# Performance work log

Measured on AMD Instinct MI355X. Metric: run time of the kernel, lower is better.

Reference implementation:

```python
import jax, jax.numpy as jnp
import numpy as np

# dims
B, S, H = 2, 256, 1024          # batch, global seq, global hidden
BH, NH = 384, 8                  # byte_hidden, num heads
HD = BH // NH                    # head dim = 48
P = 4                            # num_global_proj (seed byte positions)
S_C = 12                         # byte decode steps (= target.shape[2])
L = 4                            # num_byte_decoder_layers
V = 258                          # byte vocab (256 bytes + pad 256 + eos 257)
T = P + S_C
EOS = 257
SCALE = 1.0 / np.sqrt(HD)


def setup_inputs() -> dict:
    key = jax.random.key(0)
    ks = jax.random.split(key, 12)
    w = lambda k, shp: jax.random.normal(k, shp, jnp.float32) * 0.02
    return {
        "x": jax.random.normal(ks[0], (B, S, H), jnp.float32),
        "target": jax.random.randint(ks[1], (B, S, S_C), 0, V),
        "Wproj": w(ks[2], (H, P * BH)),
        "attn_norm": jnp.ones((L, BH), jnp.float32),
        "Wq": w(ks[3], (L, BH, BH)),
        "Wk": w(ks[4], (L, BH, BH)),
        "Wv": w(ks[5], (L, BH, BH)),
        "Wo": w(ks[6], (L, BH, BH)),
        "ffn_norm": jnp.ones((L, BH), jnp.float32),
        "W1": w(ks[7], (L, BH, 4 * BH)),
        "W2": w(ks[8], (L, 4 * BH, BH)),
        "Wlm": w(ks[9], (BH, V)),
    }


def _rms(x, g):
    return x * jax.lax.rsqrt(jnp.mean(x * x, -1, keepdims=True) + 1e-5) * g


def _block(x, kc, vc, pos, an, Wq, Wk, Wv, Wo, fn, W1, W2, causal):
    # x: [N, Lq, BH]; kc/vc: [N, T, NH, HD] KV caches; pos: static write offset
    N, Lq, _ = x.shape
    h = _rms(x, an)
    q = (h @ Wq).reshape(N, Lq, NH, HD)
    k = (h @ Wk).reshape(N, Lq, NH, HD)
    v = (h @ Wv).reshape(N, Lq, NH, HD)
    kc = jax.lax.dynamic_update_slice(kc, k, (0, pos, 0, 0))
    vc = jax.lax.dynamic_update_slice(vc, v, (0, pos, 0, 0))
    nk = pos + Lq
    sc = jnp.einsum('nqhd,nkhd->nhqk', q, kc[:, :nk]) * SCALE
    if causal:
        mask = jnp.arange(nk)[None, :] <= (pos + jnp.arange(Lq))[:, None]
        sc = jnp.where(mask[None, None], sc, jnp.float32(-1e30))
    p = jax.nn.softmax(sc, axis=-1)
    o = jnp.einsum('nhqk,nkhd->nqhd', p, vc[:, :nk]).reshape(N, Lq, BH)
    x = x + o @ Wo
    x = x + jax.nn.gelu(_rms(x, fn) @ W1, approximate=False) @ W2
    return x, kc, vc


def _forward(x, Wproj, attn_norm, Wq, Wk, Wv, Wo, ffn_norm, W1, W2, Wlm):
    N = B * S
    x0 = (x.reshape(N, H) @ Wproj).reshape(N, P, BH)
    x_out = jnp.zeros((N, T, BH), x0.dtype).at[:, :P].set(x0)
    kc = [jnp.zeros((N, T, NH, HD), x0.dtype) for _ in range(L)]
    vc = [jnp.zeros((N, T, NH, HD), x0.dtype) for _ in range(L)]
    finished = jnp.zeros((N,), bool)
    for i in range(S_C):
        if i == 0:
            pos, xi, causal = 0, x_out[:, :P], True          # prefill seed bytes
        else:
            pos, xi, causal = P + i - 1, x_out[:, P + i - 1:P + i], False  # decode 1 token
        for l in range(L):
            xi, kc[l], vc[l] = _block(xi, kc[l], vc[l], pos,
                                      attn_norm[l], Wq[l], Wk[l], Wv[l], Wo[l],
                                      ffn_norm[l], W1[l], W2[l], causal)
        gen = xi[:, -1]                                       # [N, BH]
        unf = ~finished
        # scatter only unfinished streams back (finished stay zero, as in torch)
        x_out = x_out.at[:, P + i].set(jnp.where(unf[:, None], gen, jnp.float32(0.0)))
        finished = finished | (unf & (jnp.argmax(gen, -1) == EOS))
    return x_out.reshape(B, S, T, BH)[:, :, P:, :] @ Wlm      # [B,S,S_C,V]


def reference(x, target, Wproj, attn_norm, Wq, Wk, Wv, Wo, ffn_norm, W1, W2, Wlm):
    del target  # only sets S_c (static here)
    return _forward(x, Wproj, attn_norm, Wq, Wk, Wv, Wo, ffn_norm, W1, W2, Wlm)
```

## Files before the change

kernel.cpp:

```cpp
#include <hip/hip_runtime.h>
#include <hip/hip_bf16.h>


constexpr int H_IN  = 1024;
constexpr int BH    = 384;
constexpr int NH    = 8;
constexpr int HD    = 48;
constexpr int PP    = 4;
constexpr int S_CNT = 12;
constexpr int NL    = 4;
constexpr int NV    = 258;
constexpr int TT    = 16;
constexpr int NSEQ  = 512;
constexpr int EOS_I = 257;
constexpr int NTH   = 768;
constexpr float RSCALE = 0.14433756729740646f;

typedef _Float16 h2 __attribute__((ext_vector_type(2)));
typedef _Float16 h8 __attribute__((ext_vector_type(8)));

union W16 { h8 v8; h2 h[4]; _Float16 e[8]; };

template<int N> struct IC { static constexpr int value = N; };

__device__ __forceinline__ float fdot2(h2 a, h2 b, float c) {
#if __has_builtin(__builtin_amdgcn_fdot2)
  return __builtin_amdgcn_fdot2(a, b, c, false);
#else
  return c + (float)a.x * (float)b.x + (float)a.y * (float)b.y;
#endif
}

__global__ __launch_bounds__(256)
void pack8_kernel(const float* __restrict__ src, const float* __restrict__ g,
                  h8* __restrict__ dst, int C) {
  int c  = blockIdx.x * 256 + threadIdx.x;
  int j8 = blockIdx.y;
  if (c < C) {
    h8 v;
    #pragma unroll
    for (int r = 0; r < 8; r++) {
      int row = 8 * j8 + r;
      float s = g ? g[row] : 1.0f;
      v[r] = (_Float16)(src[(size_t)row * C + c] * s);
    }
    dst[(size_t)j8 * C + c] = v;
  }
}

__global__ __launch_bounds__(NTH)
void decoder_kernel(const float* __restrict__ x,
                    const h8* __restrict__ Wproj8,
                    const h8* __restrict__ Wq8,
                    const h8* __restrict__ Wk8,
                    const h8* __restrict__ Wv8,
                    const h8* __restrict__ Wo8,
                    const h8* __restrict__ W18,
                    const h8* __restrict__ W28,
                    const h8* __restrict__ Wlm8,
                    float* __restrict__ out,
                    _Float16* __restrict__ kbuf,
                    _Float16* __restrict__ vbuf)
{
  __shared__ float xs[2][4][BH];
  __shared__ __align__(16) _Float16 xh[2][4][BH];
  __shared__ __align__(16) _Float16 qh[2][4][BH];
  __shared__ __align__(16) _Float16 oh[2][4][BH];
  __shared__ float sc[2][NH][4][TT];
  __shared__ __align__(16) union Scr {
    float qkvp[3][2][4][BH];
    float wop[2][4][BH];
    struct { __align__(16) _Float16 f1h[2][4][4*BH];
             float w2p[2][4][BH]; } ffn;
    __align__(16) _Float16 xin[2][H_IN];
  } scr;
  __shared__ float redsq[2][4][6];
  __shared__ float redv[12];
  __shared__ int   redi[12];
  __shared__ int   fin[2];

  const int tid = threadIdx.x;
  const int kg  = tid / BH;
  const int col = tid - kg * BH;
  const int sq  = kg;
  const int wid = tid >> 6;
  const int w6  = wid % 6;
  const int seq0 = blockIdx.x * 2;

  if (tid < 2) fin[tid] = 0;

  for (int s = 0; s < 2; s++) {
    const size_t base = (size_t)(seq0 + s) * H_IN;
    for (int j = tid; j < H_IN; j += NTH) scr.xin[s][j] = (_Float16)x[base + j];
  }
  __syncthreads();
  {
    float acc[2][2] = {};
    for (int j8 = 0; j8 < H_IN / 8; j8 += 4) {
      W16 w0[4], w1[4];
      #pragma unroll
      for (int u = 0; u < 4; u++) {
        w0[u].v8 = Wproj8[(size_t)(j8 + u) * (PP * BH) + tid];
        w1[u].v8 = Wproj8[(size_t)(j8 + u) * (PP * BH) + tid + NTH];
      }
      #pragma unroll
      for (int u = 0; u < 4; u++)
        #pragma unroll
        for (int s = 0; s < 2; s++) {
          W16 hv; hv.v8 = *(const h8*)&scr.xin[s][(j8 + u) * 8];
          #pragma unroll
          for (int r = 0; r < 4; r++) {
            acc[s][0] = fdot2(hv.h[r], w0[u].h[r], acc[s][0]);
            acc[s][1] = fdot2(hv.h[r], w1[u].h[r], acc[s][1]);
          }
        }
    }
    const int m0 = tid / BH, cc = tid - m0 * BH;
    #pragma unroll
    for (int s = 0; s < 2; s++) {
      xs[s][m0][cc]     = acc[s][0];  xh[s][m0][cc]     = (_Float16)acc[s][0];
      xs[s][m0 + 2][cc] = acc[s][1];  xh[s][m0 + 2][cc] = (_Float16)acc[s][1];
      float r0 = acc[s][0] * acc[s][0], r1 = acc[s][1] * acc[s][1];
      #pragma unroll
      for (int off = 32; off; off >>= 1) {
        r0 += __shfl_down(r0, off, 64); r1 += __shfl_down(r1, off, 64);
      }
      if ((tid & 63) == 0) { redsq[s][m0][w6] = r0; redsq[s][m0 + 2][w6] = r1; }
    }
  }
  __syncthreads();

  auto layers = [&](auto ntc, int pos, bool causal) {
    constexpr int NT = decltype(ntc)::value;
    const int nk = pos + NT;
    for (int l = 0; l < NL; l++) {
      {
        const size_t wb = ((size_t)l * 48 + kg * 24) * BH + col;
        float aq[2][NT] = {}, ak[2][NT] = {}, av[2][NT] = {};
        for (int j8 = 0; j8 < 24; j8 += 4) {
          W16 wq[4], wk[4], wv[4];
          #pragma unroll
          for (int u = 0; u < 4; u++) {
            wq[u].v8 = Wq8[wb + (size_t)(j8 + u) * BH];
            wk[u].v8 = Wk8[wb + (size_t)(j8 + u) * BH];
            wv[u].v8 = Wv8[wb + (size_t)(j8 + u) * BH];
          }
          #pragma unroll
          for (int u = 0; u < 4; u++)
            #pragma unroll
            for (int s = 0; s < 2; s++)
              #pragma unroll
              for (int tok = 0; tok < NT; tok++) {
                W16 hv; hv.v8 = *(const h8*)&xh[s][tok][(kg * 24 + j8 + u) * 8];
                #pragma unroll
                for (int r = 0; r < 4; r++) {
                  aq[s][tok] = fdot2(hv.h[r], wq[u].h[r], aq[s][tok]);
                  ak[s][tok] = fdot2(hv.h[r], wk[u].h[r], ak[s][tok]);
                  av[s][tok] = fdot2(hv.h[r], wv[u].h[r], av[s][tok]);
                }
              }
        }
        if (kg == 1) {
          #pragma unroll
          for (int s = 0; s < 2; s++)
            #pragma unroll
            for (int tok = 0; tok < NT; tok++) {
              scr.qkvp[0][s][tok][col] = aq[s][tok];
              scr.qkvp[1][s][tok][col] = ak[s][tok];
              scr.qkvp[2][s][tok][col] = av[s][tok];
            }
        }
        __syncthreads();
        if (kg == 0) {
          #pragma unroll
          for (int s = 0; s < 2; s++) {
            const size_t cb = (((size_t)(seq0 + s) * NL + l) * TT + pos) * BH + col;
            #pragma unroll
            for (int tok = 0; tok < NT; tok++) {
              float ss = redsq[s][tok][0] + redsq[s][tok][1] + redsq[s][tok][2] +
                         redsq[s][tok][3] + redsq[s][tok][4] + redsq[s][tok][5];
              float sca = rsqrtf(ss * (1.0f / BH) + 1e-5f);
              qh[s][tok][col] = (_Float16)((aq[s][tok] + scr.qkvp[0][s][tok][col]) * sca * RSCALE);
              kbuf[cb + (size_t)tok * BH] = (_Float16)((ak[s][tok] + scr.qkvp[1][s][tok][col]) * sca);
              vbuf[cb + (size_t)tok * BH] = (_Float16)((av[s][tok] + scr.qkvp[2][s][tok][col]) * sca);
            }
          }
        }
        __syncthreads();
      }
      {
        const int nu = 2 * NH * NT * nk;
        if (tid < nu) {
          int s = tid / (NH * NT * nk), r = tid % (NH * NT * nk);
          int h = r / (NT * nk); int r2 = r % (NT * nk);
          int qi = r2 / nk, j = r2 % nk;
          float d;
          if (causal && j > pos + qi) d = -1e30f;
          else {
            const h8* kp8 = (const h8*)(kbuf + (((size_t)(seq0 + s) * NL + l) * TT + j) * BH + h * HD);
            W16 kk[6];
            #pragma unroll
            for (int c = 0; c < 6; c++) kk[c].v8 = kp8[c];
            d = 0.f;
            #pragma unroll
            for (int c = 0; c < 6; c++)
              #pragma unroll
              for (int e = 0; e < 8; e++)
                d += (float)qh[s][qi][h * HD + c * 8 + e] * (float)kk[c].e[e];
          }
          sc[s][h][qi][j] = d;
        }
      }
      __syncthreads();
      {
        const int nr = 2 * NH * NT;
        if (tid < nr) {
          int s = tid / (NH * NT), r = tid % (NH * NT);
          int h = r / NT, qi = r % NT;
          float m = -3.0e38f;
          for (int j = 0; j < nk; j++) m = fmaxf(m, sc[s][h][qi][j]);
          float den = 0.f;
          for (int j = 0; j < nk; j++) {
            float e = expf(sc[s][h][qi][j] - m);
            sc[s][h][qi][j] = e; den += e;
          }
          float inv = 1.0f / den;
          for (int j = 0; j < nk; j++) sc[s][h][qi][j] *= inv;
        }
      }
      __syncthreads();
      {
        const size_t vb = (((size_t)(seq0 + sq) * NL + l) * TT) * BH + col;
        const int h = col / HD;
        #pragma unroll
        for (int tok = 0; tok < NT; tok++) {
          float acc = 0.f;
          int j = 0;
          for (; j + 4 <= nk; j += 4) {
            float v0 = (float)vbuf[vb + (size_t)(j + 0) * BH];
            float v1 = (float)vbuf[vb + (size_t)(j + 1) * BH];
            float v2 = (float)vbuf[vb + (size_t)(j + 2) * BH];
            float v3 = (float)vbuf[vb + (size_t)(j + 3) * BH];
            acc += sc[sq][h][tok][j] * v0 + sc[sq][h][tok][j+1] * v1 +
                   sc[sq][h][tok][j+2] * v2 + sc[sq][h][tok][j+3] * v3;
          }
          for (; j < nk; j++)
            acc += sc[sq][h][tok][j] * (float)vbuf[vb + (size_t)j * BH];
          oh[sq][tok][col] = (_Float16)acc;
        }
      }
      __syncthreads();
      {
        const size_t wb = ((size_t)l * 48 + kg * 24) * BH + col;
        float ao[2][NT] = {};
        for (int j8 = 0; j8 < 24; j8 += 8) {
          W16 w[8];
          #pragma unroll
          for (int u = 0; u < 8; u++) w[u].v8 = Wo8[wb + (size_t)(j8 + u) * BH];
          #pragma unroll
          for (int u = 0; u < 8; u++)
            #pragma unroll
            for (int s = 0; s < 2; s++)
              #pragma unroll
              for (int tok = 0; tok < NT; tok++) {
                W16 hv; hv.v8 = *(const h8*)&oh[s][tok][(kg * 24 + j8 + u) * 8];
                #pragma unroll
                for (int r = 0; r < 4; r++)
                  ao[s][tok] = fdot2(hv.h[r], w[u].h[r], ao[s][tok]);
              }
        }
        if (kg == 1) {
          #pragma unroll
          for (int s = 0; s < 2; s++)
            #pragma unroll
            for (int tok = 0; tok < NT; tok++) scr.wop[s][tok][col] = ao[s][tok];
        }
        __syncthreads();
        if (kg == 0) {
          #pragma unroll
          for (int s = 0; s < 2; s++)
            #pragma unroll
            for (int tok = 0; tok < NT; tok++) {
              float xn = xs[s][tok][col] + ao[s][tok] + scr.wop[s][tok][col];
              xs[s][tok][col] = xn; xh[s][tok][col] = (_Float16)xn;
              float r = xn * xn;
              #pragma unroll
              for (int off = 32; off; off >>= 1) r += __shfl_down(r, off, 64);
              if ((tid & 63) == 0) redsq[s][tok][wid] = r;
            }
        }
        __syncthreads();
      }
      {
        float a1[2][NT][2] = {};
        for (int j8 = 0; j8 < 48; j8 += 4) {
          W16 w0[4], w1[4];
          #pragma unroll
          for (int u = 0; u < 4; u++) {
            w0[u].v8 = W18[((size_t)(l * 48 + j8 + u)) * (4 * BH) + tid];
            w1[u].v8 = W18[((size_t)(l * 48 + j8 + u)) * (4 * BH) + tid + NTH];
          }
          #pragma unroll
          for (int u = 0; u < 4; u++)
            #pragma unroll
            for (int s = 0; s < 2; s++)
              #pragma unroll
              for (int t = 0; t < NT; t++) {
                W16 hv; hv.v8 = *(const h8*)&xh[s][t][(j8 + u) * 8];
                #pragma unroll
                for (int r = 0; r < 4; r++) {
                  a1[s][t][0] = fdot2(hv.h[r], w0[u].h[r], a1[s][t][0]);
                  a1[s][t][1] = fdot2(hv.h[r], w1[u].h[r], a1[s][t][1]);
                }
              }
        }
        #pragma unroll
        for (int s = 0; s < 2; s++)
          #pragma unroll
          for (int t = 0; t < NT; t++) {
            float ss = redsq[s][t][0] + redsq[s][t][1] + redsq[s][t][2] +
                       redsq[s][t][3] + redsq[s][t][4] + redsq[s][t][5];
            float sca = rsqrtf(ss * (1.0f / BH) + 1e-5f);
            float z0 = a1[s][t][0] * sca, z1 = a1[s][t][1] * sca;
            scr.ffn.f1h[s][t][tid]       = (_Float16)(0.5f * z0 * (1.0f + erff(z0 * 0.7071067811865476f)));
            scr.ffn.f1h[s][t][tid + NTH] = (_Float16)(0.5f * z1 * (1.0f + erff(z1 * 0.7071067811865476f)));
          }
        __syncthreads();
        {
          float a2[2][NT] = {};
          for (int j8 = 0; j8 < 96; j8 += 8) {
            W16 w[8];
            #pragma unroll
            for (int u = 0; u < 8; u++)
              w[u].v8 = W28[((size_t)(l * 192 + kg * 96 + j8 + u)) * BH + col];
            #pragma unroll
            for (int u = 0; u < 8; u++)
              #pragma unroll
              for (int s = 0; s < 2; s++)
                #pragma unroll
                for (int t = 0; t < NT; t++) {
                  W16 fv; fv.v8 = *(const h8*)&scr.ffn.f1h[s][t][(kg * 96 + j8 + u) * 8];
                  #pragma unroll
                  for (int r = 0; r < 4; r++)
                    a2[s][t] = fdot2(fv.h[r], w[u].h[r], a2[s][t]);
                }
          }
          if (kg == 1) {
            #pragma unroll
            for (int s = 0; s < 2; s++)
              #pragma unroll
              for (int t = 0; t < NT; t++) scr.ffn.w2p[s][t][col] = a2[s][t];
          }
          __syncthreads();
          if (kg == 0) {
            #pragma unroll
            for (int s = 0; s < 2; s++)
              #pragma unroll
              for (int t = 0; t < NT; t++) {
                float xn = xs[s][t][col] + a2[s][t] + scr.ffn.w2p[s][t][col];
                xs[s][t][col] = xn; xh[s][t][col] = (_Float16)xn;
                float r = xn * xn;
                #pragma unroll
                for (int off = 32; off; off >>= 1) r += __shfl_down(r, off, 64);
                if ((tid & 63) == 0) redsq[s][t][wid] = r;
              }
          }
          __syncthreads();
        }
      }
    }
  };

  for (int i = 0; i < S_CNT; i++) {
    int grow;
    if (i == 0) { layers(IC<4>{}, 0, true);           grow = 3; }
    else        { layers(IC<1>{}, PP + i - 1, false); grow = 0; }

    {
      float gen = xs[sq][grow][col];
      float v = gen; int idx = col;
      #pragma unroll
      for (int off = 32; off; off >>= 1) {
        float v2 = __shfl_down(v, off, 64); int i2 = __shfl_down(idx, off, 64);
        if (v2 > v || (v2 == v && i2 < idx)) { v = v2; idx = i2; }
      }
      if ((tid & 63) == 0) { redv[wid] = v; redi[wid] = idx; }
      float nxt = fin[sq] ? 0.0f : gen;
      xs[sq][0][col] = nxt; xh[sq][0][col] = (_Float16)nxt;
      float r = nxt * nxt;
      #pragma unroll
      for (int off = 32; off; off >>= 1) r += __shfl_down(r, off, 64);
      if ((tid & 63) == 0) redsq[sq][0][w6] = r;
      __syncthreads();
    }
    {
      if (col == 0) {
        const int b = sq * 6;
        float bv = redv[b]; int bi = redi[b];
        for (int w = 1; w < 6; w++)
          if (redv[b + w] > bv || (redv[b + w] == bv && redi[b + w] < bi)) {
            bv = redv[b + w]; bi = redi[b + w];
          }
        if (bi == EOS_I) fin[sq] = 1;
      }
      if (col < NV) {
        float acc = 0.f;
        for (int j8 = 0; j8 < 48; j8 += 8) {
          W16 w[8];
          #pragma unroll
          for (int u = 0; u < 8; u++) w[u].v8 = Wlm8[(size_t)(j8 + u) * NV + col];
          #pragma unroll
          for (int u = 0; u < 8; u++) {
            W16 gv; gv.v8 = *(const h8*)&xh[sq][0][(j8 + u) * 8];
            #pragma unroll
            for (int r = 0; r < 4; r++) acc = fdot2(gv.h[r], w[u].h[r], acc);
          }
        }
        out[((size_t)(seq0 + sq) * S_CNT + i) * NV + col] = acc;
      }
      __syncthreads();
    }
  }
}

extern "C" void kernel_launch(void* const* d_in, const int* in_sizes, int n_in,
                              void* d_out, int out_size, void* d_ws, size_t ws_size,
                              hipStream_t stream) {
  const float* x     = (const float*)d_in[0];
  const float* Wproj = (const float*)d_in[2];
  const float* an    = (const float*)d_in[3];
  const float* Wq    = (const float*)d_in[4];
  const float* Wk    = (const float*)d_in[5];
  const float* Wv    = (const float*)d_in[6];
  const float* Wo    = (const float*)d_in[7];
  const float* fn    = (const float*)d_in[8];
  const float* W1    = (const float*)d_in[9];
  const float* W2    = (const float*)d_in[10];
  const float* Wlm   = (const float*)d_in[11];
  float* out = (float*)d_out;
  (void)ws_size; (void)in_sizes; (void)n_in; (void)out_size;

  h8* w = (h8*)d_ws;
  const int n_proj = (H_IN / 8) * (PP * BH);
  const int n_qkvo = NL * (BH / 8) * BH;
  const int n_w1   = NL * (BH / 8) * (4 * BH);
  const int n_w2   = NL * (4 * BH / 8) * BH;
  const int n_lm   = (BH / 8) * NV;
  h8* Wproj_p = w;  w += n_proj;
  h8* Wq_p    = w;  w += n_qkvo;
  h8* Wk_p    = w;  w += n_qkvo;
  h8* Wv_p    = w;  w += n_qkvo;
  h8* Wo_p    = w;  w += n_qkvo;
  h8* W1_p    = w;  w += n_w1;
  h8* W2_p    = w;  w += n_w2;
  h8* Wlm_p   = w;  w += n_lm;
  const size_t kv_elems = (size_t)NSEQ * NL * TT * BH;
  _Float16* kbuf = (_Float16*)w;
  _Float16* vbuf = kbuf + kv_elems;

  auto pack = [&](const float* src, const float* g, h8* dst, int R, int C) {
    dim3 grid((C + 255) / 256, R / 8);
    pack8_kernel<<<grid, 256, 0, stream>>>(src, g, dst, C);
  };
  pack(Wproj, nullptr, Wproj_p, H_IN,        PP * BH);
  pack(Wq,    an,      Wq_p,    NL * BH,     BH);
  pack(Wk,    an,      Wk_p,    NL * BH,     BH);
  pack(Wv,    an,      Wv_p,    NL * BH,     BH);
  pack(Wo,    nullptr, Wo_p,    NL * BH,     BH);
  pack(W1,    fn,      W1_p,    NL * BH,     4 * BH);
  pack(W2,    nullptr, W2_p,    NL * 4 * BH, BH);
  pack(Wlm,   nullptr, Wlm_p,   BH,          NV);

  decoder_kernel<<<NSEQ / 2, NTH, 0, stream>>>(
      x, Wproj_p, Wq_p, Wk_p, Wv_p, Wo_p, W1_p, W2_p, Wlm_p, out, kbuf, vbuf);
}
```

Before: 2.422 ms.

## Double-buffer weight loads, split partial-sum epilogues, fuse decode attention softmax

Every weight-streaming GEMV loop (Wproj, QKV, Wo, W1, W2, Wlm) now software-pipelines its global loads into a two-stage register buffer, so the next chunk is fetched while the current one is multiplied. The split-K epilogues let each half-block finish one sequence instead of half the threads idling while the other half does both. For single-token decode, score computation and softmax are fused into one phase using 16-lane shuffles, which removes a barrier and the serial per-row softmax loop. The cost is higher register pressure from the doubled weight buffers and full unrolling.

After: 7.653 ms. 3.16x slower.

```diff
diff --git a/kernel.cpp b/kernel.cpp
--- a/kernel.cpp
+++ b/kernel.cpp
@@ -96,22 +96,31 @@
   __syncthreads();
   {
     float acc[2][2] = {};
-    for (int j8 = 0; j8 < H_IN / 8; j8 += 4) {
-      W16 w0[4], w1[4];
-      #pragma unroll
-      for (int u = 0; u < 4; u++) {
-        w0[u].v8 = Wproj8[(size_t)(j8 + u) * (PP * BH) + tid];
-        w1[u].v8 = Wproj8[(size_t)(j8 + u) * (PP * BH) + tid + NTH];
+    W16 b0[2][4], b1[2][4];
+    #pragma unroll
+    for (int u = 0; u < 4; u++) {
+      b0[0][u].v8 = Wproj8[(size_t)u * (PP * BH) + tid];
+      b1[0][u].v8 = Wproj8[(size_t)u * (PP * BH) + tid + NTH];
+    }
+    #pragma unroll
+    for (int c = 0; c < 32; c++) {
+      const int cur = c & 1, nxt = cur ^ 1;
+      if (c < 31) {
+        #pragma unroll
+        for (int u = 0; u < 4; u++) {
+          b0[nxt][u].v8 = Wproj8[(size_t)((c + 1) * 4 + u) * (PP * BH) + tid];
+          b1[nxt][u].v8 = Wproj8[(size_t)((c + 1) * 4 + u) * (PP * BH) + tid + NTH];
+        }
       }
       #pragma unroll
       for (int u = 0; u < 4; u++)
         #pragma unroll
         for (int s = 0; s < 2; s++) {
-          W16 hv; hv.v8 = *(const h8*)&scr.xin[s][(j8 + u) * 8];
+          W16 hv; hv.v8 = *(const h8*)&scr.xin[s][(c * 4 + u) * 8];
           #pragma unroll
           for (int r = 0; r < 4; r++) {
-            acc[s][0] = fdot2(hv.h[r], w0[u].h[r], acc[s][0]);
-            acc[s][1] = fdot2(hv.h[r], w1[u].h[r], acc[s][1]);
+            acc[s][0] = fdot2(hv.h[r], b0[cur][u].h[r], acc[s][0]);
+            acc[s][1] = fdot2(hv.h[r], b1[cur][u].h[r], acc[s][1]);
           }
         }
     }
@@ -137,13 +146,24 @@
       {
         const size_t wb = ((size_t)l * 48 + kg * 24) * BH + col;
         float aq[2][NT] = {}, ak[2][NT] = {}, av[2][NT] = {};
-        for (int j8 = 0; j8 < 24; j8 += 4) {
-          W16 wq[4], wk[4], wv[4];
-          #pragma unroll
-          for (int u = 0; u < 4; u++) {
-            wq[u].v8 = Wq8[wb + (size_t)(j8 + u) * BH];
-            wk[u].v8 = Wk8[wb + (size_t)(j8 + u) * BH];
-            wv[u].v8 = Wv8[wb + (size_t)(j8 + u) * BH];
+        W16 bq[2][4], bk[2][4], bv[2][4];
+        #pragma unroll
+        for (int u = 0; u < 4; u++) {
+          bq[0][u].v8 = Wq8[wb + (size_t)u * BH];
+          bk[0][u].v8 = Wk8[wb + (size_t)u * BH];
+          bv[0][u].v8 = Wv8[wb + (size_t)u * BH];
+        }
+        #pragma unroll
+        for (int c = 0; c < 6; c++) {
+          const int cur = c & 1, nxt = cur ^ 1;
+          if (c < 5) {
+            #pragma unroll
+            for (int u = 0; u < 4; u++) {
+              const size_t j = (size_t)((c + 1) * 4 + u) * BH;
+              bq[nxt][u].v8 = Wq8[wb + j];
+              bk[nxt][u].v8 = Wk8[wb + j];
+              bv[nxt][u].v8 = Wv8[wb + j];
+            }
           }
           #pragma unroll
           for (int u = 0; u < 4; u++)
@@ -151,84 +171,109 @@
             for (int s = 0; s < 2; s++)
               #pragma unroll
               for (int tok = 0; tok < NT; tok++) {
-                W16 hv; hv.v8 = *(const h8*)&xh[s][tok][(kg * 24 + j8 + u) * 8];
+                W16 hv; hv.v8 = *(const h8*)&xh[s][tok][(kg * 24 + c * 4 + u) * 8];
                 #pragma unroll
                 for (int r = 0; r < 4; r++) {
-                  aq[s][tok] = fdot2(hv.h[r], wq[u].h[r], aq[s][tok]);
-                  ak[s][tok] = fdot2(hv.h[r], wk[u].h[r], ak[s][tok]);
-                  av[s][tok] = fdot2(hv.h[r], wv[u].h[r], av[s][tok]);
+                  aq[s][tok] = fdot2(hv.h[r], bq[cur][u].h[r], aq[s][tok]);
+                  ak[s][tok] = fdot2(hv.h[r], bk[cur][u].h[r], ak[s][tok]);
+                  av[s][tok] = fdot2(hv.h[r], bv[cur][u].h[r], av[s][tok]);
                 }
               }
         }
-        if (kg == 1) {
-          #pragma unroll
-          for (int s = 0; s < 2; s++)
-            #pragma unroll
-            for (int tok = 0; tok < NT; tok++) {
-              scr.qkvp[0][s][tok][col] = aq[s][tok];
-              scr.qkvp[1][s][tok][col] = ak[s][tok];
-              scr.qkvp[2][s][tok][col] = av[s][tok];
-            }
-        }
-        __syncthreads();
-        if (kg == 0) {
-          #pragma unroll
-          for (int s = 0; s < 2; s++) {
-            const size_t cb = (((size_t)(seq0 + s) * NL + l) * TT + pos) * BH + col;
-            #pragma unroll
-            for (int tok = 0; tok < NT; tok++) {
-              float ss = redsq[s][tok][0] + redsq[s][tok][1] + redsq[s][tok][2] +
-                         redsq[s][tok][3] + redsq[s][tok][4] + redsq[s][tok][5];
-              float sca = rsqrtf(ss * (1.0f / BH) + 1e-5f);
-              qh[s][tok][col] = (_Float16)((aq[s][tok] + scr.qkvp[0][s][tok][col]) * sca * RSCALE);
-              kbuf[cb + (size_t)tok * BH] = (_Float16)((ak[s][tok] + scr.qkvp[1][s][tok][col]) * sca);
-              vbuf[cb + (size_t)tok * BH] = (_Float16)((av[s][tok] + scr.qkvp[2][s][tok][col]) * sca);
-            }
-          }
-        }
-        __syncthreads();
-      }
-      {
-        const int nu = 2 * NH * NT * nk;
-        if (tid < nu) {
-          int s = tid / (NH * NT * nk), r = tid % (NH * NT * nk);
-          int h = r / (NT * nk); int r2 = r % (NT * nk);
-          int qi = r2 / nk, j = r2 % nk;
-          float d;
-          if (causal && j > pos + qi) d = -1e30f;
-          else {
+        {
+          const int so = kg ^ 1;
+          #pragma unroll
+          for (int tok = 0; tok < NT; tok++) {
+            scr.qkvp[0][so][tok][col] = aq[so][tok];
+            scr.qkvp[1][so][tok][col] = ak[so][tok];
+            scr.qkvp[2][so][tok][col] = av[so][tok];
+          }
+        }
+        __syncthreads();
+        {
+          const int s = kg;
+          const size_t cb = (((size_t)(seq0 + s) * NL + l) * TT + pos) * BH + col;
+          #pragma unroll
+          for (int tok = 0; tok < NT; tok++) {
+            float ss = redsq[s][tok][0] + redsq[s][tok][1] + redsq[s][tok][2] +
+                       redsq[s][tok][3] + redsq[s][tok][4] + redsq[s][tok][5];
+            float sca = rsqrtf(ss * (1.0f / BH) + 1e-5f);
+            qh[s][tok][col] = (_Float16)((aq[s][tok] + scr.qkvp[0][s][tok][col]) * sca * RSCALE);
+            kbuf[cb + (size_t)tok * BH] = (_Float16)((ak[s][tok] + scr.qkvp[1][s][tok][col]) * sca);
+            vbuf[cb + (size_t)tok * BH] = (_Float16)((av[s][tok] + scr.qkvp[2][s][tok][col]) * sca);
+          }
+        }
+        __syncthreads();
+      }
+      if constexpr (NT == 1) {
+        if (tid < 2 * NH * TT) {
+          const int s = tid >> 7, r = tid & 127, h = r >> 4, j = r & 15;
+          float d = -1e30f;
+          if (j < nk) {
             const h8* kp8 = (const h8*)(kbuf + (((size_t)(seq0 + s) * NL + l) * TT + j) * BH + h * HD);
-            W16 kk[6];
-            #pragma unroll
-            for (int c = 0; c < 6; c++) kk[c].v8 = kp8[c];
             d = 0.f;
             #pragma unroll
-            for (int c = 0; c < 6; c++)
-              #pragma unroll
-              for (int e = 0; e < 8; e++)
-                d += (float)qh[s][qi][h * HD + c * 8 + e] * (float)kk[c].e[e];
-          }
-          sc[s][h][qi][j] = d;
-        }
-      }
-      __syncthreads();
-      {
-        const int nr = 2 * NH * NT;
-        if (tid < nr) {
-          int s = tid / (NH * NT), r = tid % (NH * NT);
-          int h = r / NT, qi = r % NT;
-          float m = -3.0e38f;
-          for (int j = 0; j < nk; j++) m = fmaxf(m, sc[s][h][qi][j]);
-          float den = 0.f;
-          for (int j = 0; j < nk; j++) {
-            float e = expf(sc[s][h][qi][j] - m);
-            sc[s][h][qi][j] = e; den += e;
-          }
-          float inv = 1.0f / den;
-          for (int j = 0; j < nk; j++) sc[s][h][qi][j] *= inv;
-        }
-      }
-      __syncthreads();
+            for (int c6 = 0; c6 < 6; c6++) {
+              W16 kk, qq;
+              kk.v8 = kp8[c6];
+              qq.v8 = *(const h8*)&qh[s][0][h * HD + c6 * 8];
+              #pragma unroll
+              for (int rr = 0; rr < 4; rr++) d = fdot2(qq.h[rr], kk.h[rr], d);
+            }
+          }
+          float m = d;
+          #pragma unroll
+          for (int off = 8; off; off >>= 1) m = fmaxf(m, __shfl_xor(m, off, 16));
+          float e = expf(d - m);
+          float den = e;
+          #pragma unroll
+          for (int off = 8; off; off >>= 1) den += __shfl_xor(den, off, 16);
+          sc[s][h][0][j] = e * (1.0f / den);
+        }
+        __syncthreads();
+      } else {
+        {
+          const int nu = 2 * NH * NT * nk;
+          if (tid < nu) {
+            int s = tid / (NH * NT * nk), r = tid % (NH * NT * nk);
+            int h = r / (NT * nk); int r2 = r % (NT * nk);
+            int qi = r2 / nk, j = r2 % nk;
+            float d;
+            if (causal && j > pos + qi) d = -1e30f;
+            else {
+              const h8* kp8 = (const h8*)(kbuf + (((size_t)(seq0 + s) * NL + l) * TT + j) * BH + h * HD);
+              d = 0.f;
+              #pragma unroll
+              for (int c6 = 0; c6 < 6; c6++) {
+                W16 kk, qq;
+                kk.v8 = kp8[c6];
+                qq.v8 = *(const h8*)&qh[s][qi][h * HD + c6 * 8];
+                #pragma unroll
+                for (int rr = 0; rr < 4; rr++) d = fdot2(qq.h[rr], kk.h[rr], d);
+              }
+            }
+            sc[s][h][qi][j] = d;
+          }
+        }
+        __syncthreads();
+        {
+          const int nr = 2 * NH * NT;
+          if (tid < nr) {
+            int s = tid / (NH * NT), r = tid % (NH * NT);
+            int h = r / NT, qi = r % NT;
+            float m = -3.0e38f;
+            for (int j = 0; j < nk; j++) m = fmaxf(m, sc[s][h][qi][j]);
+            float den = 0.f;
+            for (int j = 0; j < nk; j++) {
+              float e = expf(sc[s][h][qi][j] - m);
+              sc[s][h][qi][j] = e; den += e;
+            }
+            float inv = 1.0f / den;
+            for (int j = 0; j < nk; j++) sc[s][h][qi][j] *= inv;
+          }
+        }
+        __syncthreads();
+      }
       {
         const size_t vb = (((size_t)(seq0 + sq) * NL + l) * TT) * BH + col;
         const int h = col / HD;
@@ -241,8 +286,8 @@
             float v1 = (float)vbuf[vb + (size_t)(j + 1) * BH];
             float v2 = (float)vbuf[vb + (size_t)(j + 2) * BH];
             float v3 = (float)vbuf[vb + (size_t)(j + 3) * BH];
-            acc += sc[sq][h][tok][j] * v0 + sc[sq][h][tok][j+1] * v1 +
-                   sc[sq][h][tok][j+2] * v2 + sc[sq][h][tok][j+3] * v3;
+            acc += sc[sq][h][tok][j] * v0 + sc[sq][h][tok][j + 1] * v1 +
+                   sc[sq][h][tok][j + 2] * v2 + sc[sq][h][tok][j + 3] * v3;
           }
           for (; j < nk; j++)
             acc += sc[sq][h][tok][j] * (float)vbuf[vb + (size_t)j * BH];
@@ -253,66 +298,82 @@
       {
         const size_t wb = ((size_t)l * 48 + kg * 24) * BH + col;
         float ao[2][NT] = {};
-        for (int j8 = 0; j8 < 24; j8 += 8) {
-          W16 w[8];
-          #pragma unroll
-          for (int u = 0; u < 8; u++) w[u].v8 = Wo8[wb + (size_t)(j8 + u) * BH];
+        W16 bw[2][8];
+        #pragma unroll
+        for (int u = 0; u < 8; u++) bw[0][u].v8 = Wo8[wb + (size_t)u * BH];
+        #pragma unroll
+        for (int c = 0; c < 3; c++) {
+          const int cur = c & 1, nxt = cur ^ 1;
+          if (c < 2) {
+            #pragma unroll
+            for (int u = 0; u < 8; u++)
+              bw[nxt][u].v8 = Wo8[wb + (size_t)((c + 1) * 8 + u) * BH];
+          }
           #pragma unroll
           for (int u = 0; u < 8; u++)
             #pragma unroll
             for (int s = 0; s < 2; s++)
               #pragma unroll
               for (int tok = 0; tok < NT; tok++) {
-                W16 hv; hv.v8 = *(const h8*)&oh[s][tok][(kg * 24 + j8 + u) * 8];
+                W16 hv; hv.v8 = *(const h8*)&oh[s][tok][(kg * 24 + c * 8 + u) * 8];
                 #pragma unroll
                 for (int r = 0; r < 4; r++)
-                  ao[s][tok] = fdot2(hv.h[r], w[u].h[r], ao[s][tok]);
+                  ao[s][tok] = fdot2(hv.h[r], bw[cur][u].h[r], ao[s][tok]);
               }
         }
-        if (kg == 1) {
-          #pragma unroll
-          for (int s = 0; s < 2; s++)
-            #pragma unroll
-            for (int tok = 0; tok < NT; tok++) scr.wop[s][tok][col] = ao[s][tok];
-        }
-        __syncthreads();
-        if (kg == 0) {
-          #pragma unroll
-          for (int s = 0; s < 2; s++)
-            #pragma unroll
-            for (int tok = 0; tok < NT; tok++) {
-              float xn = xs[s][tok][col] + ao[s][tok] + scr.wop[s][tok][col];
-              xs[s][tok][col] = xn; xh[s][tok][col] = (_Float16)xn;
-              float r = xn * xn;
-              #pragma unroll
-              for (int off = 32; off; off >>= 1) r += __shfl_down(r, off, 64);
-              if ((tid & 63) == 0) redsq[s][tok][wid] = r;
-            }
+        {
+          const int so = kg ^ 1;
+          #pragma unroll
+          for (int tok = 0; tok < NT; tok++) scr.wop[so][tok][col] = ao[so][tok];
+        }
+        __syncthreads();
+        {
+          const int s = kg;
+          #pragma unroll
+          for (int tok = 0; tok < NT; tok++) {
+            float xn = xs[s][tok][col] + ao[s][tok] + scr.wop[s][tok][col];
+            xs[s][tok][col] = xn; xh[s][tok][col] = (_Float16)xn;
+            float r = xn * xn;
+            #pragma unroll
+            for (int off = 32; off; off >>= 1) r += __shfl_down(r, off, 64);
+            if ((tid & 63) == 0) redsq[s][tok][w6] = r;
+          }
         }
         __syncthreads();
       }
       {
         float a1[2][NT][2] = {};
-        for (int j8 = 0; j8 < 48; j8 += 4) {
-          W16 w0[4], w1[4];
+        {
+          W16 c0[2][4], c1[2][4];
           #pragma unroll
           for (int u = 0; u < 4; u++) {
-            w0[u].v8 = W18[((size_t)(l * 48 + j8 + u)) * (4 * BH) + tid];
-            w1[u].v8 = W18[((size_t)(l * 48 + j8 + u)) * (4 * BH) + tid + NTH];
-          }
-          #pragma unroll
-          for (int u = 0; u < 4; u++)
-            #pragma unroll
-            for (int s = 0; s < 2; s++)
-              #pragma unroll
-              for (int t = 0; t < NT; t++) {
-                W16 hv; hv.v8 = *(const h8*)&xh[s][t][(j8 + u) * 8];
+            c0[0][u].v8 = W18[((size_t)(l * 48 + u)) * (4 * BH) + tid];
+            c1[0][u].v8 = W18[((size_t)(l * 48 + u)) * (4 * BH) + tid + NTH];
+          }
+          #pragma unroll
+          for (int c = 0; c < 12; c++) {
+            const int cur = c & 1, nxt = cur ^ 1;
+            if (c < 11) {
+              #pragma unroll
+              for (int u = 0; u < 4; u++) {
+                c0[nxt][u].v8 = W18[((size_t)(l * 48 + (c + 1) * 4 + u)) * (4 * BH) + tid];
+                c1[nxt][u].v8 = W18[((size_t)(l * 48 + (c + 1) * 4 + u)) * (4 * BH) + tid + NTH];
+              }
+            }
+            #pragma unroll
+            for (int u = 0; u < 4; u++)
+              #pragma unroll
+              for (int s = 0; s < 2; s++)
                 #pragma unroll
-                for (int r = 0; r < 4; r++) {
-                  a1[s][t][0] = fdot2(hv.h[r], w0[u].h[r], a1[s][t][0]);
-                  a1[s][t][1] = fdot2(hv.h[r], w1[u].h[r], a1[s][t][1]);
+                for (int t = 0; t < NT; t++) {
+                  W16 hv; hv.v8 = *(const h8*)&xh[s][t][(c * 4 + u) * 8];
+                  #pragma unroll
+                  for (int r = 0; r < 4; r++) {
+                    a1[s][t][0] = fdot2(hv.h[r], c0[cur][u].h[r], a1[s][t][0]);
+                    a1[s][t][1] = fdot2(hv.h[r], c1[cur][u].h[r], a1[s][t][1]);
+                  }
                 }
-              }
+          }
         }
         #pragma unroll
         for (int s = 0; s < 2; s++)
@@ -328,42 +389,47 @@
         __syncthreads();
         {
           float a2[2][NT] = {};
-          for (int j8 = 0; j8 < 96; j8 += 8) {
-            W16 w[8];
-            #pragma unroll
-            for (int u = 0; u < 8; u++)
-              w[u].v8 = W28[((size_t)(l * 192 + kg * 96 + j8 + u)) * BH + col];
+          W16 bw[2][8];
+          #pragma unroll
+          for (int u = 0; u < 8; u++)
+            bw[0][u].v8 = W28[((size_t)(l * 192 + kg * 96 + u)) * BH + col];
+          #pragma unroll
+          for (int c = 0; c < 12; c++) {
+            const int cur = c & 1, nxt = cur ^ 1;
+            if (c < 11) {
+              #pragma unroll
+              for (int u = 0; u < 8; u++)
+                bw[nxt][u].v8 = W28[((size_t)(l * 192 + kg * 96 + (c + 1) * 8 + u)) * BH + col];
+            }
             #pragma unroll
             for (int u = 0; u < 8; u++)
               #pragma unroll
               for (int s = 0; s < 2; s++)
                 #pragma unroll
                 for (int t = 0; t < NT; t++) {
-                  W16 fv; fv.v8 = *(const h8*)&scr.ffn.f1h[s][t][(kg * 96 + j8 + u) * 8];
+                  W16 fv; fv.v8 = *(const h8*)&scr.ffn.f1h[s][t][(kg * 96 + c * 8 + u) * 8];
                   #pragma unroll
                   for (int r = 0; r < 4; r++)
-                    a2[s][t] = fdot2(fv.h[r], w[u].h[r], a2[s][t]);
+                    a2[s][t] = fdot2(fv.h[r], bw[cur][u].h[r], a2[s][t]);
                 }
           }
-          if (kg == 1) {
-            #pragma unroll
-            for (int s = 0; s < 2; s++)
-              #pragma unroll
-              for (int t = 0; t < NT; t++) scr.ffn.w2p[s][t][col] = a2[s][t];
+          {
+            const int so = kg ^ 1;
+            #pragma unroll
+            for (int t = 0; t < NT; t++) scr.ffn.w2p[so][t][col] = a2[so][t];
           }
           __syncthreads();
-          if (kg == 0) {
-            #pragma unroll
-            for (int s = 0; s < 2; s++)
-              #pragma unroll
-              for (int t = 0; t < NT; t++) {
-                float xn = xs[s][t][col] + a2[s][t] + scr.ffn.w2p[s][t][col];
-                xs[s][t][col] = xn; xh[s][t][col] = (_Float16)xn;
-                float r = xn * xn;
-                #pragma unroll
-                for (int off = 32; off; off >>= 1) r += __shfl_down(r, off, 64);
-                if ((tid & 63) == 0) redsq[s][t][wid] = r;
-              }
+          {
+            const int s = kg;
+            #pragma unroll
+            for (int t = 0; t < NT; t++) {
+              float xn = xs[s][t][col] + a2[s][t] + scr.ffn.w2p[s][t][col];
+              xs[s][t][col] = xn; xh[s][t][col] = (_Float16)xn;
+              float r = xn * xn;
+              #pragma unroll
+              for (int off = 32; off; off >>= 1) r += __shfl_down(r, off, 64);
+              if ((tid & 63) == 0) redsq[s][t][w6] = r;
+            }
           }
           __syncthreads();
         }
@@ -405,15 +471,22 @@
       }
       if (col < NV) {
         float acc = 0.f;
-        for (int j8 = 0; j8 < 48; j8 += 8) {
-          W16 w[8];
-          #pragma unroll
-          for (int u = 0; u < 8; u++) w[u].v8 = Wlm8[(size_t)(j8 + u) * NV + col];
+        W16 bw[2][8];
+        #pragma unroll
+        for (int u = 0; u < 8; u++) bw[0][u].v8 = Wlm8[(size_t)u * NV + col];
+        #pragma unroll
+        for (int c = 0; c < 6; c++) {
+          const int cur = c & 1, nxt = cur ^ 1;
+          if (c < 5) {
+            #pragma unroll
+            for (int u = 0; u < 8; u++)
+              bw[nxt][u].v8 = Wlm8[(size_t)((c + 1) * 8 + u) * NV + col];
+          }
           #pragma unroll
           for (int u = 0; u < 8; u++) {
-            W16 gv; gv.v8 = *(const h8*)&xh[sq][0][(j8 + u) * 8];
-            #pragma unroll
-            for (int r = 0; r < 4; r++) acc = fdot2(gv.h[r], w[u].h[r], acc);
+            W16 gv; gv.v8 = *(const h8*)&xh[sq][0][(c * 8 + u) * 8];
+            #pragma unroll
+            for (int r = 0; r < 4; r++) acc = fdot2(gv.h[r], bw[cur][u].h[r], acc);
           }
         }
         out[((size_t)(seq0 + sq) * S_CNT + i) * NV + col] = acc;
```
